# Performance work log

Measured on AMD Instinct MI355X. Metric: run time of the kernel, lower is better.

The kernel has to match this reference:

```python
import jax, jax.numpy as jnp
import numpy as np

B, T, C, H = 2, 2048, 1024, 16
HD = C // H
MAX_WAVELENGTH = 10000.0


def apply_rope(x, positions):
    # x: [B, H, T, HD], positions: [T]
    fraction = 2.0 * jnp.arange(HD // 2, dtype=jnp.float32) / HD
    timescale = MAX_WAVELENGTH ** fraction  # [HD//2]
    sinusoid = positions[:, None] / timescale[None, :]  # [T, HD//2]
    sin = jnp.sin(sinusoid)
    cos = jnp.cos(sinusoid)
    first, second = jnp.split(x, 2, axis=-1)
    out = jnp.concatenate(
        [first * cos - second * sin, second * cos + first * sin], axis=-1
    )
    return out.astype(x.dtype)


def setup_inputs() -> dict:
    key = jax.random.key(0)
    k1, k2, k3 = jax.random.split(key, 3)
    x = jax.random.normal(k1, (B, T, C), dtype=jnp.float32)
    w_attn = jax.random.normal(k2, (C, 3 * C), dtype=jnp.float32) * 0.02
    b_attn = jnp.zeros((3 * C,), dtype=jnp.float32)
    w_proj = jax.random.normal(k3, (C, C), dtype=jnp.float32) * 0.02
    b_proj = jnp.zeros((C,), dtype=jnp.float32)
    return {"x": x, "w_attn": w_attn, "b_attn": b_attn,
            "w_proj": w_proj, "b_proj": b_proj}


def reference(x, w_attn, b_attn, w_proj, b_proj):
    b, t, c = x.shape
    qkv = x @ w_attn + b_attn  # [B, T, 3C]
    q, k, v = jnp.split(qkv, 3, axis=-1)
    q = q.reshape(b, t, H, HD).transpose(0, 2, 1, 3)  # [B, H, T, HD]
    k = k.reshape(b, t, H, HD).transpose(0, 2, 1, 3)
    v = v.reshape(b, t, H, HD).transpose(0, 2, 1, 3)
    positions = jnp.arange(t, dtype=x.dtype)
    q = apply_rope(q, positions)
    k = apply_rope(k, positions)
    att = jnp.einsum('bhqd,bhkd->bhqk', q, k) * (1.0 / jnp.sqrt(HD))
    causal = jnp.tril(jnp.ones((t, t), dtype=bool))
    att = jnp.where(causal, att, jnp.finfo(att.dtype).min)
    att = jax.nn.softmax(att, axis=-1)
    y = jnp.einsum('bhqk,bhkd->bhqd', att, v)
    y = y.transpose(0, 2, 1, 3).reshape(b, t, c)
    return y @ w_proj + b_proj
```

## Files before the change

### kernel.cpp

```cpp
#include <hip/hip_runtime.h>
#include <hip/hip_bf16.h>


typedef __attribute__((ext_vector_type(8))) short short8;
typedef __attribute__((ext_vector_type(4))) float floatx4;

__device__ __forceinline__ unsigned short f2bf(float f) {
    union { float f; unsigned int u; } v; v.f = f;
    unsigned int r = v.u + 0x7FFFu + ((v.u >> 16) & 1u);
    return (unsigned short)(r >> 16);
}

__device__ __forceinline__ unsigned int pk2bf(float a, float b) {
    union { float f; unsigned int u; } ua, ub;
    ua.f = a; ub.f = b;
    return __builtin_amdgcn_perm(ub.u + 0x8000u, ua.u + 0x8000u, 0x07060302u);
}

__device__ __forceinline__ unsigned int cvtpk(float a, float b) {
    unsigned int r;
    asm("v_cvt_pk_bf16_f32 %0, %1, %2" : "=v"(r) : "v"(a), "v"(b));
    return r;
}

__device__ __forceinline__ void gld16(const void* g, void* l) {
    __builtin_amdgcn_global_load_lds(
        (const __attribute__((address_space(1))) unsigned int*)g,
        (__attribute__((address_space(3))) unsigned int*)l, 16, 0, 0);
}

__device__ __forceinline__ void transpose_body(
    const float* __restrict__ in, unsigned short* __restrict__ out,
    int R, int NC, int bx, int by, int tid,
    unsigned short (*tile)[68]) {
    int r0 = by * 64, c0 = bx * 64;
    int c4 = (tid & 15) * 4, rr = tid >> 4;
#pragma unroll
    for (int i = 0; i < 4; i++) {
        int row = rr + i * 16;
        float4 v = *(const float4*)&in[(size_t)(r0 + row) * NC + c0 + c4];
        ushort4 o;
        o.x = f2bf(v.x); o.y = f2bf(v.y); o.z = f2bf(v.z); o.w = f2bf(v.w);
        *(ushort4*)&tile[row][c4] = o;
    }
    __syncthreads();
    int col = tid & 63, rr2 = tid >> 6;
#pragma unroll
    for (int i = 0; i < 16; i++) {
        int orow = rr2 + i * 4;
        out[(size_t)(c0 + orow) * R + r0 + col] = tile[col][orow];
    }
}

__global__ __launch_bounds__(256) void prep(
    const float* __restrict__ x,
    const float* __restrict__ w_attn,
    const float* __restrict__ w_proj,
    unsigned short* __restrict__ x_bf,
    unsigned short* __restrict__ wTa,
    unsigned short* __restrict__ wTp,
    float2* __restrict__ tab) {
    __shared__ unsigned short tile[64][68];
    int bid = blockIdx.x;
    int tid = threadIdx.x;
    if (bid < 4096) {
        int i = bid * 256 + tid;
        float4 v = ((const float4*)x)[i];
        ushort4 o;
        o.x = f2bf(v.x); o.y = f2bf(v.y); o.z = f2bf(v.z); o.w = f2bf(v.w);
        ((ushort4*)x_bf)[i] = o;
    } else if (bid < 4864) {
        int t = bid - 4096;
        transpose_body(w_attn, wTa, 1024, 3072, t % 48, t / 48, tid, tile);
    } else if (bid < 5120) {
        int t = bid - 4864;
        transpose_body(w_proj, wTp, 1024, 1024, t & 15, t >> 4, tid, tile);
    } else {
        int i = (bid - 5120) * 256 + tid;
        int t = i >> 5, d = i & 31;
        float inv_ts = exp2f(-0.41524101186092036f * (float)d);
        float ang = (float)t * inv_ts;
        tab[i] = make_float2(sinf(ang), cosf(ang));
    }
}

__global__ __launch_bounds__(256) void gemm_qkv(
    const unsigned short* __restrict__ A,
    const unsigned short* __restrict__ BT,
    const float* __restrict__ bias,
    const float2* __restrict__ tab,
    unsigned short* __restrict__ qT,
    unsigned short* __restrict__ kT,
    unsigned short* __restrict__ vT) {
    __shared__ __align__(16) unsigned short smem[32768];
    int tid = threadIdx.x;
    int lane = tid & 63;
    int w = tid >> 6;
    int wx = w & 1, wy = w >> 1;
    int l16 = lane & 15, quad = lane >> 4;
    int lin = blockIdx.x;
    int swz = (lin & 7) * 96 + (lin >> 3);
    int m0 = (swz / 24) * 128;
    int n0 = (swz % 24) * 128;
    int x = l16 & 7;
    int lr = lane >> 3;
    int gc = (lane & 7) ^ lr;

    floatx4 acc[4][4];
#pragma unroll
    for (int mi = 0; mi < 4; mi++)
#pragma unroll
        for (int ni = 0; ni < 4; ni++)
            acc[mi][ni] = (floatx4){0.f, 0.f, 0.f, 0.f};

    auto stage = [&](int bsel, int k0) {
        unsigned short* as = smem + bsel * 16384;
        unsigned short* bs = as + 8192;
#pragma unroll
        for (int i = 0; i < 4; i++) {
            int seg = w * 4 + i;
            int row = seg * 8 + lr;
            gld16(A + (size_t)(m0 + row) * 1024 + k0 + gc * 8, &as[seg * 512]);
            gld16(BT + (size_t)(n0 + row) * 1024 + k0 + gc * 8, &bs[seg * 512]);
        }
    };

    auto compute = [&](int bsel) {
        const unsigned short* as = smem + bsel * 16384;
        const unsigned short* bs = as + 8192;
#pragma unroll
        for (int kk = 0; kk < 2; kk++) {
            short8 af[4], bf[4];
#pragma unroll
            for (int mi = 0; mi < 4; mi++) {
                int r = wy * 64 + mi * 16 + l16;
                af[mi] = *(const short8*)&as[r * 64 + (((kk << 2) | quad) ^ x) * 8];
            }
#pragma unroll
            for (int ni = 0; ni < 4; ni++) {
                int r = wx * 64 + ni * 16 + l16;
                bf[ni] = *(const short8*)&bs[r * 64 + (((kk << 2) | quad) ^ x) * 8];
            }
#pragma unroll
            for (int mi = 0; mi < 4; mi++)
#pragma unroll
                for (int ni = 0; ni < 4; ni++)
                    acc[mi][ni] = __builtin_amdgcn_mfma_f32_16x16x32_bf16(
                        af[mi], bf[ni], acc[mi][ni], 0, 0, 0);
        }
    };

    stage(0, 0);
    int cur = 0;
    for (int k0 = 0; k0 < 960; k0 += 64) {
        stage(cur ^ 1, k0 + 64);
        asm volatile("s_waitcnt vmcnt(8)" ::: "memory");
        __builtin_amdgcn_s_barrier();
        compute(cur);
        asm volatile("s_waitcnt lgkmcnt(0)" ::: "memory");
        __builtin_amdgcn_s_barrier();
        cur ^= 1;
    }
    asm volatile("s_waitcnt vmcnt(0)" ::: "memory");
    __builtin_amdgcn_s_barrier();
    compute(cur);
    __syncthreads();

    int region = n0 >> 10;
    int b = m0 >> 11;
    float b0 = bias[n0 + wx * 64 + l16];
    float b1 = bias[n0 + wx * 64 + 16 + l16];
    float b2 = bias[n0 + wx * 64 + 32 + l16];
    float b3 = bias[n0 + wx * 64 + 48 + l16];

    if (region < 2) {
        unsigned short* qk = region ? kT : qT;
        float scale = region ? 1.0f : 0.18033688011112042f;
        unsigned short* lq = smem;
#pragma unroll
        for (int mi = 0; mi < 4; mi++)
#pragma unroll
            for (int r = 0; r < 4; r++) {
                int tl = wy * 64 + mi * 16 + quad * 4 + r;
                int t = (m0 & 2047) + tl;
                float2 sc0 = tab[t * 32 + l16];
                float2 sc1 = tab[t * 32 + 16 + l16];
                float v1 = acc[mi][0][r] + b0, v2 = acc[mi][2][r] + b2;
                float w1 = acc[mi][1][r] + b1, w2 = acc[mi][3][r] + b3;
                unsigned short* orow = lq + tl * 136 + wx * 64;
                orow[l16]      = f2bf((v1 * sc0.y - v2 * sc0.x) * scale);
                orow[l16 + 32] = f2bf((v2 * sc0.y + v1 * sc0.x) * scale);
                orow[l16 + 16] = f2bf((w1 * sc1.y - w2 * sc1.x) * scale);
                orow[l16 + 48] = f2bf((w2 * sc1.y + w1 * sc1.x) * scale);
            }
        __syncthreads();
        int c8 = tid & 7;
        int hl = (tid >> 3) & 1;
        int tl0 = tid >> 4;
        int h = ((n0 & 1023) >> 6) + hl;
        unsigned short* ob = qk + (size_t)(b * 16 + h) * 2048 * 64;
#pragma unroll
        for (int p = 0; p < 8; p++) {
            int tl = p * 16 + tl0;
            int t = (m0 & 2047) + tl;
            short8 val = *(const short8*)&lq[tl * 136 + hl * 64 + c8 * 8];
            *(short8*)&ob[(size_t)t * 64 + c8 * 8] = val;
        }
    } else {
#pragma unroll
        for (int mi = 0; mi < 4; mi++)
#pragma unroll
            for (int ni = 0; ni < 4; ni++) {
                int d_loc = wx * 64 + ni * 16 + l16;
                int t_base = wy * 64 + mi * 16 + quad * 4;
                float bv = (ni == 0) ? b0 : (ni == 1) ? b1 : (ni == 2) ? b2 : b3;
                uint2 pk;
                pk.x = pk2bf(acc[mi][ni][0] + bv, acc[mi][ni][1] + bv);
                pk.y = pk2bf(acc[mi][ni][2] + bv, acc[mi][ni][3] + bv);
                int e = d_loc * 128 + (t_base ^ ((d_loc & 15) << 3));
                *(uint2*)&smem[e] = pk;
            }
        __syncthreads();
        int d_r = tid >> 1, half = tid & 1;
        int cv = (n0 - 2048) + d_r;
        int hh = cv >> 6, dd = cv & 63;
        int fofs = (d_r & 15) << 3;
        size_t vbase = ((size_t)(b * 16 + hh) * 64 + dd) * 2048 + (m0 & 2047);
#pragma unroll
        for (int c = 0; c < 8; c++) {
            int tc = half * 64 + c * 8;
            short8 val = *(const short8*)&smem[d_r * 128 + (tc ^ fofs)];
            *(short8*)&vT[vbase + tc] = val;
        }
    }
}

__global__ __launch_bounds__(256) void gemm_proj(
    const unsigned short* __restrict__ A,
    const unsigned short* __restrict__ BT,
    const float* __restrict__ bias,
    float* __restrict__ out) {
    __shared__ __align__(16) unsigned short smem[24576];
    int lane = threadIdx.x & 63;
    int w = threadIdx.x >> 6;
    int wx = w & 1, wy = w >> 1;
    int l16 = lane & 15, quad = lane >> 4;
    int lin = blockIdx.x;
    int swz = (lin & 7) * 64 + (lin >> 3);
    int m0 = (swz >> 4) * 128;
    int n0 = (swz & 15) * 64;
    int x = l16 & 7;
    int lr = lane >> 3;
    int gc = (lane & 7) ^ lr;

    floatx4 acc[4][2];
#pragma unroll
    for (int mi = 0; mi < 4; mi++)
#pragma unroll
        for (int ni = 0; ni < 2; ni++)
            acc[mi][ni] = (floatx4){0.f, 0.f, 0.f, 0.f};

    auto stage = [&](int bsel, int k0) {
        unsigned short* as = smem + bsel * 12288;
        unsigned short* bs = as + 8192;
#pragma unroll
        for (int i = 0; i < 6; i++) {
            int seg = w * 6 + i;
            if (seg < 16) {
                int row = seg * 8 + lr;
                gld16(A + (size_t)(m0 + row) * 1024 + k0 + gc * 8, &as[seg * 512]);
            } else {
                int s2 = seg - 16;
                int row = s2 * 8 + lr;
                gld16(BT + (size_t)(n0 + row) * 1024 + k0 + gc * 8, &bs[s2 * 512]);
            }
        }
    };

    auto compute = [&](int bsel) {
        const unsigned short* as = smem + bsel * 12288;
        const unsigned short* bs = as + 8192;
#pragma unroll
        for (int kk = 0; kk < 2; kk++) {
            short8 af[4], bf[2];
#pragma unroll
            for (int mi = 0; mi < 4; mi++) {
                int r = wy * 64 + mi * 16 + l16;
                af[mi] = *(const short8*)&as[r * 64 + (((kk << 2) | quad) ^ x) * 8];
            }
#pragma unroll
            for (int ni = 0; ni < 2; ni++) {
                int r = wx * 32 + ni * 16 + l16;
                bf[ni] = *(const short8*)&bs[r * 64 + (((kk << 2) | quad) ^ x) * 8];
            }
#pragma unroll
            for (int mi = 0; mi < 4; mi++)
#pragma unroll
                for (int ni = 0; ni < 2; ni++)
                    acc[mi][ni] = __builtin_amdgcn_mfma_f32_16x16x32_bf16(
                        af[mi], bf[ni], acc[mi][ni], 0, 0, 0);
        }
    };

    stage(0, 0);
    int cur = 0;
    for (int k0 = 0; k0 < 960; k0 += 64) {
        stage(cur ^ 1, k0 + 64);
        asm volatile("s_waitcnt vmcnt(6)" ::: "memory");
        __builtin_amdgcn_s_barrier();
        compute(cur);
        asm volatile("s_waitcnt lgkmcnt(0)" ::: "memory");
        __builtin_amdgcn_s_barrier();
        cur ^= 1;
    }
    asm volatile("s_waitcnt vmcnt(0)" ::: "memory");
    __builtin_amdgcn_s_barrier();
    compute(cur);

#pragma unroll
    for (int mi = 0; mi < 4; mi++)
#pragma unroll
        for (int ni = 0; ni < 2; ni++) {
            int row = m0 + wy * 64 + mi * 16 + quad * 4;
            int col = n0 + wx * 32 + ni * 16 + l16;
            float bv = bias[col];
#pragma unroll
            for (int r = 0; r < 4; r++)
                out[(size_t)(row + r) * 1024 + col] = acc[mi][ni][r] + bv;
        }
}

__global__ __launch_bounds__(256) void attn5(
    const unsigned short* __restrict__ qT,
    const unsigned short* __restrict__ kT,
    const unsigned short* __restrict__ vT,
    unsigned short* __restrict__ y) {
    __shared__ __align__(16) unsigned short kbuf[2][64 * 64];
    __shared__ __align__(16) unsigned short vbuf[2][64 * 64];
    __shared__ __align__(16) unsigned short pl[4][16 * 72];
    int lane = threadIdx.x & 63;
    int w = threadIdx.x >> 6;
    int l16 = lane & 15, quad = lane >> 4;
    int blk = blockIdx.x;
    int t = 31 - (blk >> 5);
    int bh = blk & 31;
    int b = bh >> 4, h = bh & 15;
    int q0 = t * 64 + w * 16;
    const unsigned short* qp = qT + (size_t)bh * 2048 * 64;
    unsigned short* plw = pl[w];
    int x = l16 & 7;

    short8 qf0 = *(const short8*)(qp + (size_t)(q0 + l16) * 64 + quad * 8);
    short8 qf1 = *(const short8*)(qp + (size_t)(q0 + l16) * 64 + 32 + quad * 8);

    short8 ones;
#pragma unroll
    for (int j = 0; j < 8; j++) ones[j] = (short)0x3F80;

    floatx4 acc[4];
#pragma unroll
    for (int ni = 0; ni < 4; ni++) acc[ni] = (floatx4){0.f, 0.f, 0.f, 0.f};
    floatx4 accl = (floatx4){0.f, 0.f, 0.f, 0.f};

    int lr8 = lane >> 3, l8 = lane & 7;
    const unsigned short* sp[4];
    unsigned short* ld0[4];
    int gstep;
    if (w < 2) {
        const unsigned short* kp = kT + (size_t)bh * 2048 * 64;
#pragma unroll
        for (int i = 0; i < 4; i++) {
            int seg = w * 4 + i;
            int row = seg * 8 + lr8;
            int c = l8 ^ (row & 7);
            sp[i] = kp + (size_t)row * 64 + c * 8;
            ld0[i] = &kbuf[0][seg * 512];
        }
        gstep = 4096;
    } else {
        const unsigned short* vp = vT + (size_t)bh * 64 * 2048;
#pragma unroll
        for (int i = 0; i < 4; i++) {
            int s = (w - 2) * 4 + i;
            int d = s * 8 + lr8;
            int c = l8 ^ (d & 7);
            sp[i] = vp + (size_t)d * 2048 + c * 8;
            ld0[i] = &vbuf[0][s * 512];
        }
        gstep = 64;
    }

    auto stage = [&](int bi) {
#pragma unroll
        for (int i = 0; i < 4; i++) {
            gld16(sp[i], ld0[i] + bi * 4096);
            sp[i] += gstep;
        }
    };

    int L = t + 1;
    int query = q0 + l16;
    stage(0);
    int cur = 0;
    for (int it = 0; it < L; it++) {
        if (it + 1 < L) {
            stage(cur ^ 1);
            asm volatile("s_waitcnt vmcnt(4)" ::: "memory");
        } else {
            asm volatile("s_waitcnt vmcnt(0)" ::: "memory");
        }
        __builtin_amdgcn_s_barrier();
        const unsigned short* kb = kbuf[cur];
        const unsigned short* vb = vbuf[cur];
        bool diag = (it == t);
        floatx4 s4[4];
        __builtin_amdgcn_s_setprio(1);
#pragma unroll
        for (int c = 0; c < 4; c++) {
            int r = c * 16 + l16;
            short8 kf0 = *(const short8*)&kb[r * 64 + ((quad) ^ x) * 8];
            short8 kf1 = *(const short8*)&kb[r * 64 + ((quad | 4) ^ x) * 8];
            floatx4 z = (floatx4){0.f, 0.f, 0.f, 0.f};
            z = __builtin_amdgcn_mfma_f32_16x16x32_bf16(kf0, qf0, z, 0, 0, 0);
            z = __builtin_amdgcn_mfma_f32_16x16x32_bf16(kf1, qf1, z, 0, 0, 0);
            s4[c] = z;
        }
        __builtin_amdgcn_s_setprio(0);
        int j0 = it * 64;
#pragma unroll
        for (int c = 0; c < 4; c++) {
            float p[4];
#pragma unroll
            for (int r = 0; r < 4; r++) {
                float e = __builtin_amdgcn_exp2f(s4[c][r]);
                if (diag) {
                    int key = j0 + c * 16 + quad * 4 + r;
                    e = (key <= query) ? e : 0.f;
                }
                p[r] = e;
            }
            uint2 pk;
            pk.x = cvtpk(p[0], p[1]);
            pk.y = cvtpk(p[2], p[3]);
            *(uint2*)&plw[l16 * 72 + c * 16 + quad * 4] = pk;
        }
        short8 pa0 = *(const short8*)&plw[l16 * 72 + quad * 8];
        short8 pa1 = *(const short8*)&plw[l16 * 72 + 32 + quad * 8];
        __builtin_amdgcn_s_setprio(1);
        accl = __builtin_amdgcn_mfma_f32_16x16x32_bf16(pa0, ones, accl, 0, 0, 0);
        accl = __builtin_amdgcn_mfma_f32_16x16x32_bf16(pa1, ones, accl, 0, 0, 0);
#pragma unroll
        for (int ni = 0; ni < 4; ni++) {
            int d = ni * 16 + l16;
            short8 vf0 = *(const short8*)&vb[d * 64 + ((quad) ^ x) * 8];
            short8 vf1 = *(const short8*)&vb[d * 64 + ((quad | 4) ^ x) * 8];
            acc[ni] = __builtin_amdgcn_mfma_f32_16x16x32_bf16(pa0, vf0, acc[ni], 0, 0, 0);
            acc[ni] = __builtin_amdgcn_mfma_f32_16x16x32_bf16(pa1, vf1, acc[ni], 0, 0, 0);
        }
        __builtin_amdgcn_s_setprio(0);
        asm volatile("s_waitcnt lgkmcnt(0)" ::: "memory");
        __builtin_amdgcn_s_barrier();
        cur ^= 1;
    }

    float inv[4];
#pragma unroll
    for (int r = 0; r < 4; r++) inv[r] = 1.f / accl[r];
#pragma unroll
    for (int ni = 0; ni < 4; ni++)
#pragma unroll
        for (int r = 0; r < 4; r++) {
            int tr = q0 + quad * 4 + r;
            y[((size_t)(b * 2048 + tr)) * 1024 + h * 64 + ni * 16 + l16] =
                f2bf(acc[ni][r] * inv[r]);
        }
}

extern "C" void kernel_launch(void* const* d_in, const int* in_sizes, int n_in,
                              void* d_out, int out_size, void* d_ws, size_t ws_size,
                              hipStream_t stream) {
    const float* x      = (const float*)d_in[0];
    const float* w_attn = (const float*)d_in[1];
    const float* b_attn = (const float*)d_in[2];
    const float* w_proj = (const float*)d_in[3];
    const float* b_proj = (const float*)d_in[4];
    float* out = (float*)d_out;

    char* ws = (char*)d_ws;
    unsigned short* x_bf = (unsigned short*)ws;
    unsigned short* wTa  = (unsigned short*)(ws + (8ull << 20));
    unsigned short* wTp  = (unsigned short*)(ws + (14ull << 20));
    unsigned short* qTb  = (unsigned short*)(ws + (16ull << 20));
    unsigned short* kTb  = (unsigned short*)(ws + (24ull << 20));
    unsigned short* vTb  = (unsigned short*)(ws + (32ull << 20));
    float2*         tab  = (float2*)(ws + (40ull << 20));
    unsigned short* y_bf = x_bf;

    prep<<<5376, 256, 0, stream>>>(x, w_attn, w_proj, x_bf, wTa, wTp, tab);
    gemm_qkv<<<768, 256, 0, stream>>>(x_bf, wTa, b_attn, tab, qTb, kTb, vTb);
    attn5<<<1024, 256, 0, stream>>>(qTb, kTb, vTb, y_bf);
    gemm_proj<<<512, 256, 0, stream>>>(y_bf, wTp, b_proj, out);
}
```

Measured before the change: 165.5 us.

## Halve QKV GEMM K-tile and LDS footprint, split epilogue into two passes

The QKV projection GEMM now stages K-tiles of 32 instead of 64, which halves its shared-memory buffer. The LDS swizzle pattern for the narrower rows changes to match. The RoPE epilogue writes Q and K through LDS in two 64-row halves so it fits the smaller buffer. The aim is more resident blocks per CU for latency hiding, at the cost of twice as many loop iterations and barriers, plus extra epilogue syncs.

```diff
diff --git a/kernel.cpp b/kernel.cpp
--- a/kernel.cpp
+++ b/kernel.cpp
@@ -92,7 +92,7 @@
     unsigned short* __restrict__ qT,
     unsigned short* __restrict__ kT,
     unsigned short* __restrict__ vT) {
-    __shared__ __align__(16) unsigned short smem[32768];
+    __shared__ __align__(16) unsigned short smem[16384];
     int tid = threadIdx.x;
     int lane = tid & 63;
     int w = tid >> 6;
@@ -102,9 +102,8 @@
     int swz = (lin & 7) * 96 + (lin >> 3);
     int m0 = (swz / 24) * 128;
     int n0 = (swz % 24) * 128;
-    int x = l16 & 7;
-    int lr = lane >> 3;
-    int gc = (lane & 7) ^ lr;
+    int l2 = lane >> 2;
+    int c4p = lane & 3;
 
     floatx4 acc[4][4];
 #pragma unroll
@@ -114,47 +113,45 @@
             acc[mi][ni] = (floatx4){0.f, 0.f, 0.f, 0.f};
 
     auto stage = [&](int bsel, int k0) {
-        unsigned short* as = smem + bsel * 16384;
-        unsigned short* bs = as + 8192;
-#pragma unroll
-        for (int i = 0; i < 4; i++) {
-            int seg = w * 4 + i;
-            int row = seg * 8 + lr;
-            gld16(A + (size_t)(m0 + row) * 1024 + k0 + gc * 8, &as[seg * 512]);
-            gld16(BT + (size_t)(n0 + row) * 1024 + k0 + gc * 8, &bs[seg * 512]);
+        unsigned short* as = smem + bsel * 8192;
+        unsigned short* bs = as + 4096;
+#pragma unroll
+        for (int i = 0; i < 2; i++) {
+            int seg = w * 2 + i;
+            int row = seg * 16 + l2;
+            int gk = (c4p ^ ((row >> 1) & 3)) * 8;
+            gld16(A + (size_t)(m0 + row) * 1024 + k0 + gk, &as[seg * 512]);
+            gld16(BT + (size_t)(n0 + row) * 1024 + k0 + gk, &bs[seg * 512]);
         }
     };
 
     auto compute = [&](int bsel) {
-        const unsigned short* as = smem + bsel * 16384;
-        const unsigned short* bs = as + 8192;
-#pragma unroll
-        for (int kk = 0; kk < 2; kk++) {
-            short8 af[4], bf[4];
-#pragma unroll
-            for (int mi = 0; mi < 4; mi++) {
-                int r = wy * 64 + mi * 16 + l16;
-                af[mi] = *(const short8*)&as[r * 64 + (((kk << 2) | quad) ^ x) * 8];
-            }
-#pragma unroll
-            for (int ni = 0; ni < 4; ni++) {
-                int r = wx * 64 + ni * 16 + l16;
-                bf[ni] = *(const short8*)&bs[r * 64 + (((kk << 2) | quad) ^ x) * 8];
-            }
-#pragma unroll
-            for (int mi = 0; mi < 4; mi++)
-#pragma unroll
-                for (int ni = 0; ni < 4; ni++)
-                    acc[mi][ni] = __builtin_amdgcn_mfma_f32_16x16x32_bf16(
-                        af[mi], bf[ni], acc[mi][ni], 0, 0, 0);
-        }
+        const unsigned short* as = smem + bsel * 8192;
+        const unsigned short* bs = as + 4096;
+        short8 af[4], bf[4];
+#pragma unroll
+        for (int mi = 0; mi < 4; mi++) {
+            int r = wy * 64 + mi * 16 + l16;
+            af[mi] = *(const short8*)&as[r * 32 + (quad ^ ((r >> 1) & 3)) * 8];
+        }
+#pragma unroll
+        for (int ni = 0; ni < 4; ni++) {
+            int r = wx * 64 + ni * 16 + l16;
+            bf[ni] = *(const short8*)&bs[r * 32 + (quad ^ ((r >> 1) & 3)) * 8];
+        }
+#pragma unroll
+        for (int mi = 0; mi < 4; mi++)
+#pragma unroll
+            for (int ni = 0; ni < 4; ni++)
+                acc[mi][ni] = __builtin_amdgcn_mfma_f32_16x16x32_bf16(
+                    af[mi], bf[ni], acc[mi][ni], 0, 0, 0);
     };
 
     stage(0, 0);
     int cur = 0;
-    for (int k0 = 0; k0 < 960; k0 += 64) {
-        stage(cur ^ 1, k0 + 64);
-        asm volatile("s_waitcnt vmcnt(8)" ::: "memory");
+    for (int k0 = 0; k0 < 992; k0 += 32) {
+        stage(cur ^ 1, k0 + 32);
+        asm volatile("s_waitcnt vmcnt(4)" ::: "memory");
         __builtin_amdgcn_s_barrier();
         compute(cur);
         asm volatile("s_waitcnt lgkmcnt(0)" ::: "memory");
@@ -177,34 +174,40 @@
         unsigned short* qk = region ? kT : qT;
         float scale = region ? 1.0f : 0.18033688011112042f;
         unsigned short* lq = smem;
-#pragma unroll
-        for (int mi = 0; mi < 4; mi++)
-#pragma unroll
-            for (int r = 0; r < 4; r++) {
-                int tl = wy * 64 + mi * 16 + quad * 4 + r;
-                int t = (m0 & 2047) + tl;
-                float2 sc0 = tab[t * 32 + l16];
-                float2 sc1 = tab[t * 32 + 16 + l16];
-                float v1 = acc[mi][0][r] + b0, v2 = acc[mi][2][r] + b2;
-                float w1 = acc[mi][1][r] + b1, w2 = acc[mi][3][r] + b3;
-                unsigned short* orow = lq + tl * 136 + wx * 64;
-                orow[l16]      = f2bf((v1 * sc0.y - v2 * sc0.x) * scale);
-                orow[l16 + 32] = f2bf((v2 * sc0.y + v1 * sc0.x) * scale);
-                orow[l16 + 16] = f2bf((w1 * sc1.y - w2 * sc1.x) * scale);
-                orow[l16 + 48] = f2bf((w2 * sc1.y + w1 * sc1.x) * scale);
-            }
-        __syncthreads();
         int c8 = tid & 7;
         int hl = (tid >> 3) & 1;
         int tl0 = tid >> 4;
         int h = ((n0 & 1023) >> 6) + hl;
         unsigned short* ob = qk + (size_t)(b * 16 + h) * 2048 * 64;
 #pragma unroll
-        for (int p = 0; p < 8; p++) {
-            int tl = p * 16 + tl0;
-            int t = (m0 & 2047) + tl;
-            short8 val = *(const short8*)&lq[tl * 136 + hl * 64 + c8 * 8];
-            *(short8*)&ob[(size_t)t * 64 + c8 * 8] = val;
+        for (int hf = 0; hf < 2; hf++) {
+            if (wy == hf) {
+#pragma unroll
+                for (int mi = 0; mi < 4; mi++)
+#pragma unroll
+                    for (int r = 0; r < 4; r++) {
+                        int lr_ = mi * 16 + quad * 4 + r;
+                        int t = (m0 & 2047) + hf * 64 + lr_;
+                        float2 sc0 = tab[t * 32 + l16];
+                        float2 sc1 = tab[t * 32 + 16 + l16];
+                        float v1 = acc[mi][0][r] + b0, v2 = acc[mi][2][r] + b2;
+                        float w1 = acc[mi][1][r] + b1, w2 = acc[mi][3][r] + b3;
+                        unsigned short* orow = lq + lr_ * 136 + wx * 64;
+                        orow[l16]      = f2bf((v1 * sc0.y - v2 * sc0.x) * scale);
+                        orow[l16 + 32] = f2bf((v2 * sc0.y + v1 * sc0.x) * scale);
+                        orow[l16 + 16] = f2bf((w1 * sc1.y - w2 * sc1.x) * scale);
+                        orow[l16 + 48] = f2bf((w2 * sc1.y + w1 * sc1.x) * scale);
+                    }
+            }
+            __syncthreads();
+#pragma unroll
+            for (int p = 0; p < 4; p++) {
+                int rl = p * 16 + tl0;
+                int t = (m0 & 2047) + hf * 64 + rl;
+                short8 val = *(const short8*)&lq[rl * 136 + hl * 64 + c8 * 8];
+                *(short8*)&ob[(size_t)t * 64 + c8 * 8] = val;
+            }
+            __syncthreads();
         }
     } else {
 #pragma unroll
```

Result: slower. 177.4 us (+7.2%).
